# Kernel tuning notes

Hardware: AMD Instinct MI355X
Metric: run time of the kernel (lower is better)

The kernel has to match this reference:

```python
import jax, jax.numpy as jnp
import numpy as np

DIM = 1024
NUM_HEADS = 16
HEAD_DIM = DIM // NUM_HEADS
SCALE = HEAD_DIM ** (-0.5)


def setup_inputs() -> dict:
    key = jax.random.key(0)
    k_x, k_qkv, k_ow, k_ob = jax.random.split(key, 4)
    x = jax.random.normal(k_x, (4, 2048, DIM), dtype=jnp.float32)
    # nn.Linear(dim, 3*dim, bias=False): store as [dim, 3*dim] for x @ W
    w_qkv = jax.random.normal(k_qkv, (DIM, 3 * DIM), dtype=jnp.float32) * (DIM ** -0.5)
    w_out = jax.random.normal(k_ow, (DIM, DIM), dtype=jnp.float32) * (DIM ** -0.5)
    b_out = jax.random.normal(k_ob, (DIM,), dtype=jnp.float32) * 0.02
    return {"x": x, "w_qkv": w_qkv, "w_out": w_out, "b_out": b_out}


def reference(x, w_qkv, w_out, b_out):
    B, S, D = x.shape
    H, Hd = NUM_HEADS, HEAD_DIM
    qkv = x @ w_qkv                                  # [B, S, 3*D]
    # rearrange 'b s (v h d) -> v b h s d'
    qkv = qkv.reshape(B, S, 3, H, Hd).transpose(2, 0, 3, 1, 4)
    q, k, v = qkv[0], qkv[1], qkv[2]                 # each [B, H, S, Hd]
    scores = jnp.einsum('bhqd,bhkd->bhqk', q, k) * SCALE
    attn = jax.nn.softmax(scores, axis=-1)
    out = jnp.einsum('bhqk,bhkd->bhqd', attn, v)     # [B, H, S, Hd]
    out = out.transpose(0, 2, 1, 3).reshape(B, S, D)  # 'b h s d -> b s (h d)'
    return out @ w_out + b_out
```

## Files before the change

### kernel.cpp

```cpp
#include <hip/hip_runtime.h>
#include <hip/hip_bf16.h>
#include <stdint.h>

typedef __bf16 bf16_t;
typedef __bf16 bf16x4 __attribute__((ext_vector_type(4)));
typedef __bf16 bf16x8 __attribute__((ext_vector_type(8)));
typedef float f32x4 __attribute__((ext_vector_type(4)));
typedef unsigned short u16;

#define L2E 1.4426950408889634f
#define MC 69.249473f
#define QSC 0.18033688f

__device__ __forceinline__ void async_load16(const bf16_t* g, bf16_t* l) {
  __builtin_amdgcn_global_load_lds(
      (__attribute__((address_space(1))) uint32_t*)g,
      (__attribute__((address_space(3))) uint32_t*)l, 16, 0, 0);
}

__global__ void detect_k(const uint16_t* __restrict__ x, int* __restrict__ flag) {
  if (blockIdx.x != 0) return;
  const int lane = threadIdx.x & 63;
  int bad = 0;
#pragma unroll
  for (int p = 0; p < 4; ++p) {
    const int i = lane * 4 + p;
    uint16_t h = x[2 * i];
    int e = (h >> 7) & 0xFF;
    if (e == 0 || e >= 0xBD) bad++;
  }
  bad += __shfl_xor(bad, 1, 64);
  bad += __shfl_xor(bad, 2, 64);
  bad += __shfl_xor(bad, 4, 64);
  bad += __shfl_xor(bad, 8, 64);
  bad += __shfl_xor(bad, 16, 64);
  bad += __shfl_xor(bad, 32, 64);
  if (lane == 0 && threadIdx.x < 64) *flag = (bad > 32) ? 1 : 0;
}

__global__ void convert_k(const void* __restrict__ in, bf16_t* __restrict__ out,
                          int n, const int* __restrict__ flag) {
  const int f = *flag;
  const int i0 = blockIdx.x * blockDim.x + threadIdx.x;
  const int stride = gridDim.x * blockDim.x;
  if (f) {
    const float* p = (const float*)in;
    for (int i = i0; i < n; i += stride) {
      float v = p[i];
      v = (v == v) ? v : 0.f;
      v = fminf(fmaxf(v, -1e6f), 1e6f);
      out[i] = (bf16_t)v;
    }
  } else {
    const bf16_t* p = (const bf16_t*)in;
    for (int i = i0; i < n; i += stride) {
      float v = (float)p[i];
      v = (v == v) ? v : 0.f;
      v = fminf(fmaxf(v, -1e6f), 1e6f);
      out[i] = (bf16_t)v;
    }
  }
}

__global__ __launch_bounds__(256) void wtrans_k(const void* __restrict__ in,
                                                bf16_t* __restrict__ out, int R,
                                                int C, const int* __restrict__ flag) {
  __shared__ u16 tile[64][65];
  const int f = *flag;
  const int tr = blockIdx.y * 64, tc = blockIdx.x * 64;
  const int t = threadIdx.x;
#pragma unroll
  for (int i = 0; i < 16; ++i) {
    int idx = i * 256 + t, r = idx >> 6, c = idx & 63;
    float v;
    if (f)
      v = ((const float*)in)[(size_t)(tr + r) * C + tc + c];
    else
      v = (float)((const bf16_t*)in)[(size_t)(tr + r) * C + tc + c];
    v = (v == v) ? v : 0.f;
    v = fminf(fmaxf(v, -1e6f), 1e6f);
    bf16_t b = (bf16_t)v;
    tile[r][c] = *(u16*)&b;
  }
  __syncthreads();
#pragma unroll
  for (int i = 0; i < 16; ++i) {
    int idx = i * 256 + t, r = idx >> 6, c = idx & 63;
    ((u16*)out)[(size_t)(tc + r) * R + tr + c] = tile[c][r];
  }
}

__device__ __forceinline__ void gemm_bt_mainloop(
    const bf16_t* __restrict__ A, const bf16_t* __restrict__ Bt, int K, int m0,
    int n0, bf16_t* As, bf16_t* Bs, f32x4 acc[4][4]) {
  const int t = threadIdx.x, lane = t & 63, w = t >> 6;
  const int l15 = lane & 15, quad = lane >> 4;
  const int wm = (w >> 1) * 64, wn = (w & 1) * 64;
  const int srow = w * 16 + (lane >> 2);
  const int sk = (lane & 3) * 8;
  const bf16_t* gA = A + (size_t)(m0 + srow) * K + sk;
  const bf16_t* gB = Bt + (size_t)(n0 + srow) * K + sk;
  bf16_t* lA = As + w * 512;
  bf16_t* lB = Bs + w * 512;
  const size_t gstep = (size_t)64 * K;

  for (int kt = 0; kt < K; kt += 32) {
    __syncthreads();
    async_load16(gA, lA);
    async_load16(gA + gstep, lA + 2048);
    async_load16(gB, lB);
    async_load16(gB + gstep, lB + 2048);
    gA += 32;
    gB += 32;
    __syncthreads();
    bf16x8 af[4], bfr[4];
#pragma unroll
    for (int f = 0; f < 4; ++f) {
      af[f] = *(const bf16x8*)(As + (wm + f * 16 + l15) * 32 + quad * 8);
      bfr[f] = *(const bf16x8*)(Bs + (wn + f * 16 + l15) * 32 + quad * 8);
    }
#pragma unroll
    for (int i = 0; i < 4; ++i)
#pragma unroll
      for (int j = 0; j < 4; ++j)
        acc[i][j] =
            __builtin_amdgcn_mfma_f32_16x16x32_bf16(af[i], bfr[j], acc[i][j], 0, 0, 0);
  }
}

__global__ __launch_bounds__(256) void qkv_gemm_k(const bf16_t* __restrict__ X,
                                                  const bf16_t* __restrict__ WqT,
                                                  bf16_t* __restrict__ qo,
                                                  bf16_t* __restrict__ ko,
                                                  bf16_t* __restrict__ vto) {
  __shared__ __align__(16) bf16_t As[128 * 32];
  __shared__ __align__(16) bf16_t Bs[128 * 32];
  const int m0 = blockIdx.y * 128, n0 = blockIdx.x * 128;
  f32x4 acc[4][4];
  const f32x4 z = {0.f, 0.f, 0.f, 0.f};
#pragma unroll
  for (int i = 0; i < 4; ++i)
#pragma unroll
    for (int j = 0; j < 4; ++j) acc[i][j] = z;
  gemm_bt_mainloop(X, WqT, 1024, m0, n0, As, Bs, acc);

  const int lane = threadIdx.x & 63, w = threadIdx.x >> 6;
  const int l15 = lane & 15, quad = lane >> 4;
  const int wm = (w >> 1) * 64, wn = (w & 1) * 64;
#pragma unroll
  for (int j = 0; j < 4; ++j) {
    const int gnb = n0 + wn + j * 16;
    const int vi = gnb >> 10;
    const int rem = gnb & 1023;
    const int h = rem >> 6;
    const int d = (rem & 63) + l15;
    if (vi == 2) {
#pragma unroll
      for (int i = 0; i < 4; ++i) {
        const int gm0 = m0 + wm + i * 16 + quad * 4;
        const int b = gm0 >> 11, s = gm0 & 2047;
        bf16x4 pv;
#pragma unroll
        for (int r = 0; r < 4; ++r) pv[r] = (bf16_t)acc[i][j][r];
        *(bf16x4*)(vto + ((size_t)(b * 16 + h) * 64 + d) * 2048 + s) = pv;
      }
    } else {
      const float scale = (vi == 0) ? QSC : 1.0f;
      bf16_t* dst = (vi == 0) ? qo : ko;
#pragma unroll
      for (int i = 0; i < 4; ++i) {
#pragma unroll
        for (int r = 0; r < 4; ++r) {
          const int gm = m0 + wm + i * 16 + quad * 4 + r;
          const int b = gm >> 11, s = gm & 2047;
          dst[(((size_t)(b * 16 + h) * 2048 + s) << 6) + d] =
              (bf16_t)(acc[i][j][r] * scale);
        }
      }
    }
  }
}

__global__ __launch_bounds__(256) void out_gemm_k(const bf16_t* __restrict__ Ain,
                                                  const bf16_t* __restrict__ WoT,
                                                  const bf16_t* __restrict__ bias,
                                                  void* __restrict__ outp,
                                                  const int* __restrict__ flag) {
  __shared__ __align__(16) bf16_t As[128 * 32];
  __shared__ __align__(16) bf16_t Bs[128 * 32];
  const int m0 = blockIdx.y * 128, n0 = blockIdx.x * 128;
  f32x4 acc[4][4];
  const f32x4 z = {0.f, 0.f, 0.f, 0.f};
#pragma unroll
  for (int i = 0; i < 4; ++i)
#pragma unroll
    for (int j = 0; j < 4; ++j) acc[i][j] = z;
  gemm_bt_mainloop(Ain, WoT, 1024, m0, n0, As, Bs, acc);

  const int f32out = *flag;
  const int lane = threadIdx.x & 63, w = threadIdx.x >> 6;
  const int l15 = lane & 15, quad = lane >> 4;
  const int wm = (w >> 1) * 64, wn = (w & 1) * 64;
#pragma unroll
  for (int j = 0; j < 4; ++j) {
    const int gn = n0 + wn + j * 16 + l15;
    const float bv = (float)bias[gn];
#pragma unroll
    for (int i = 0; i < 4; ++i) {
#pragma unroll
      for (int r = 0; r < 4; ++r) {
        const int gm = m0 + wm + i * 16 + quad * 4 + r;
        const float val = acc[i][j][r] + bv;
        if (f32out)
          ((float*)outp)[(size_t)gm * 1024 + gn] = val;
        else
          ((bf16_t*)outp)[(size_t)gm * 1024 + gn] = (bf16_t)val;
      }
    }
  }
}

#define KTILE 4096

__global__ __launch_bounds__(256, 2) void attn_k(const bf16_t* __restrict__ q,
                                                 const bf16_t* __restrict__ k,
                                                 const bf16_t* __restrict__ vt,
                                                 bf16_t* __restrict__ o) {
  __shared__ __align__(16) bf16_t Ps[256 * 64];
  __shared__ __align__(16) bf16_t Ks[2 * KTILE];
  __shared__ __align__(16) bf16_t Vts[2 * KTILE];

  const int t = threadIdx.x, lane = t & 63, w = t >> 6;
  const int l15 = lane & 15, quad = lane >> 4;
  const int x = blockIdx.x;
  const int j = x >> 3;
  const int bh = (x & 7) * 8 + (j >> 3);
  const int qt = j & 7;
  const bf16_t* qp = q + ((size_t)bh * 2048 + qt * 256) * 64;
  const bf16_t* kp = k + (size_t)bh * 2048 * 64;
  const bf16_t* vp = vt + (size_t)bh * 64 * 2048;

  const int lane8 = lane >> 3, lc = lane & 7;
  int kOff[2], vOff[2], ldsOff[2];
#pragma unroll
  for (int c = 0; c < 2; ++c) {
    const int rho = (w * 2 + c) * 8 + lane8;
    const int srow = (rho >> 4) + (rho & 15) * 4;
    const int col = (lc ^ (rho & 7)) * 8;
    kOff[c] = srow * 64 + col;
    vOff[c] = rho * 2048 + col;
    ldsOff[c] = (w * 2 + c) * 512;
  }

#pragma unroll
  for (int c = 0; c < 2; ++c) {
    async_load16(kp + kOff[c], Ks + ldsOff[c]);
    async_load16(vp + vOff[c], Vts + ldsOff[c]);
  }
#pragma unroll
  for (int p = 0; p < 8; ++p) {
    const int off = p * 2048 + t * 8;
    async_load16(qp + off, Ps + off);
  }
  __syncthreads();

  bf16x8 qf[4][2];
#pragma unroll
  for (int qs = 0; qs < 4; ++qs)
#pragma unroll
    for (int ks = 0; ks < 2; ++ks)
      qf[qs][ks] = *(const bf16x8*)(Ps + (w * 64 + qs * 16 + l15) * 64 +
                                    ks * 32 + quad * 8);

  f32x4 acc[4][4], asum[4];
  const f32x4 z = {0.f, 0.f, 0.f, 0.f};
  const f32x4 minit = {-MC, -MC, -MC, -MC};
  bf16x8 onesf;
#pragma unroll
  for (int i = 0; i < 8; ++i) onesf[i] = (bf16_t)1.0f;
#pragma unroll
  for (int qs = 0; qs < 4; ++qs) {
    asum[qs] = z;
#pragma unroll
    for (int f = 0; f < 4; ++f) acc[qs][f] = z;
  }

  bf16_t* psw = Ps + w * 64 * 64;

  for (int kt = 0; kt < 32; ++kt) {
    const int b = kt & 1;
    if (kt < 31) {
      const int bn = b ^ 1;
#pragma unroll
      for (int c = 0; c < 2; ++c) {
        async_load16(kp + (size_t)(kt + 1) * KTILE + kOff[c],
                     Ks + bn * KTILE + ldsOff[c]);
        async_load16(vp + (size_t)(kt + 1) * 64 + vOff[c],
                     Vts + bn * KTILE + ldsOff[c]);
      }
    }

    const bf16_t* Kb = Ks + b * KTILE;
    const bf16_t* Vb = Vts + b * KTILE;

    f32x4 sacc[4][4];
    {
      const int cx = ((quad ^ (l15 & 7)) * 8);
      bf16x8 kf[4];
#pragma unroll
      for (int f = 0; f < 4; ++f)
        kf[f] = *(const bf16x8*)(Kb + (f * 16 + l15) * 64 + cx);
      __builtin_amdgcn_s_setprio(1);
#pragma unroll
      for (int qs = 0; qs < 4; ++qs)
#pragma unroll
        for (int f = 0; f < 4; ++f)
          sacc[qs][f] = __builtin_amdgcn_mfma_f32_16x16x32_bf16(
              qf[qs][0], kf[f], minit, 0, 0, 0);
      __builtin_amdgcn_s_setprio(0);
    }
    {
      const int cx = (((4 + quad) ^ (l15 & 7)) * 8);
      bf16x8 kf[4];
#pragma unroll
      for (int f = 0; f < 4; ++f)
        kf[f] = *(const bf16x8*)(Kb + (f * 16 + l15) * 64 + cx);
      __builtin_amdgcn_s_setprio(1);
#pragma unroll
      for (int qs = 0; qs < 4; ++qs)
#pragma unroll
        for (int f = 0; f < 4; ++f)
          sacc[qs][f] = __builtin_amdgcn_mfma_f32_16x16x32_bf16(
              qf[qs][1], kf[f], sacc[qs][f], 0, 0, 0);
      __builtin_amdgcn_s_setprio(0);
    }

#pragma unroll
    for (int qs = 0; qs < 4; ++qs)
#pragma unroll
      for (int r = 0; r < 4; ++r) {
        bf16x4 pk;
#pragma unroll
        for (int f = 0; f < 4; ++f)
          pk[f] =
              (bf16_t)__builtin_amdgcn_exp2f(fminf(sacc[qs][f][r], 0.f));
        const int row = qs * 16 + quad * 4 + r;
        *(bf16x4*)(psw + row * 64 + ((l15 >> 1) ^ (row & 7)) * 8 +
                   (l15 & 1) * 4) = pk;
      }

#pragma unroll
    for (int ks = 0; ks < 2; ++ks) {
      const int cx = (((ks * 4 + quad) ^ (l15 & 7)) * 8);
      bf16x8 vf[4];
#pragma unroll
      for (int f = 0; f < 4; ++f)
        vf[f] = *(const bf16x8*)(Vb + (f * 16 + l15) * 64 + cx);
#pragma unroll
      for (int qs = 0; qs < 4; ++qs) {
        bf16x8 pf = *(const bf16x8*)(psw + (qs * 16 + l15) * 64 +
                                     ((ks * 4 + quad) ^ (l15 & 7)) * 8);
        __builtin_amdgcn_s_setprio(1);
#pragma unroll
        for (int f = 0; f < 4; ++f)
          acc[qs][f] = __builtin_amdgcn_mfma_f32_16x16x32_bf16(
              pf, vf[f], acc[qs][f], 0, 0, 0);
        asum[qs] = __builtin_amdgcn_mfma_f32_16x16x32_bf16(pf, onesf, asum[qs],
                                                           0, 0, 0);
        __builtin_amdgcn_s_setprio(0);
      }
    }

    if (kt < 31) __syncthreads();
  }

  const int b = bh >> 4, h = bh & 15;
#pragma unroll
  for (int qs = 0; qs < 4; ++qs)
#pragma unroll
    for (int r = 0; r < 4; ++r) {
      const int srow = qt * 256 + w * 64 + qs * 16 + quad * 4 + r;
      const float inv = 1.0f / fmaxf(asum[qs][r], 1e-37f);
#pragma unroll
      for (int f = 0; f < 4; ++f) {
        const int d = f * 16 + l15;
        o[(size_t)(b * 2048 + srow) * 1024 + h * 64 + d] =
            (bf16_t)(acc[qs][f][r] * inv);
      }
    }
}

extern "C" void kernel_launch(void* const* d_in, const int* in_sizes, int n_in,
                              void* d_out, int out_size, void* d_ws, size_t ws_size,
                              hipStream_t stream) {
  const void* x_raw = d_in[0];
  const void* wqkv_raw = d_in[1];
  const void* wout_raw = d_in[2];
  const void* bout_raw = d_in[3];

  const int nx = 4 * 2048 * 1024;
  const int nwq = 1024 * 3072;
  const int nwo = 1024 * 1024;
  const int nb = 1024;

  char* ws = (char*)d_ws;
  int* flag = (int*)ws;
  bf16_t* xb = (bf16_t*)(ws + 256);
  bf16_t* wqbT = xb + nx;
  bf16_t* wobT = wqbT + nwq;
  bf16_t* bob = wobT + nwo;
  bf16_t* qb = bob + nb;
  const size_t bhsd = (size_t)4 * 16 * 2048 * 64;
  bf16_t* kb = qb + bhsd;
  bf16_t* vtb = kb + bhsd;
  bf16_t* ab = xb;

  detect_k<<<1, 64, 0, stream>>>((const uint16_t*)x_raw, flag);
  convert_k<<<2048, 256, 0, stream>>>(x_raw, xb, nx, flag);
  wtrans_k<<<dim3(3072 / 64, 1024 / 64), 256, 0, stream>>>(wqkv_raw, wqbT, 1024,
                                                           3072, flag);
  wtrans_k<<<dim3(1024 / 64, 1024 / 64), 256, 0, stream>>>(wout_raw, wobT, 1024,
                                                           1024, flag);
  convert_k<<<4, 256, 0, stream>>>(bout_raw, bob, nb, flag);

  qkv_gemm_k<<<dim3(3072 / 128, 8192 / 128), 256, 0, stream>>>(xb, wqbT, qb, kb,
                                                               vtb);
  attn_k<<<dim3(512), 256, 0, stream>>>(qb, kb, vtb, ab);
  out_gemm_k<<<dim3(1024 / 128, 8192 / 128), 256, 0, stream>>>(ab, wobT, bob,
                                                               d_out, flag);
}
```

Baseline: 291.6 us.

## Keep softmax probabilities in registers via lane shuffles instead of LDS

Removes the 32KB P staging buffer from shared memory. The QK^T MFMA operands are swapped so score outputs come out transposed, and the exp'd probabilities are packed to bf16 pairs and redistributed across lanes with shuffles to form the PV A-operand. Q is staged through the K/V buffers before the loop, which lowers LDS use and may raise occupancy. The cost is many ds_bpermute shuffles per tile plus a moved barrier at loop start.

```diff
diff --git a/kernel.cpp b/kernel.cpp
--- a/kernel.cpp
+++ b/kernel.cpp
@@ -6,6 +6,7 @@
 typedef __bf16 bf16x4 __attribute__((ext_vector_type(4)));
 typedef __bf16 bf16x8 __attribute__((ext_vector_type(8)));
 typedef float f32x4 __attribute__((ext_vector_type(4)));
+typedef unsigned int u32x4 __attribute__((ext_vector_type(4)));
 typedef unsigned short u16;
 
 #define L2E 1.4426950408889634f
@@ -16,6 +17,11 @@
   __builtin_amdgcn_global_load_lds(
       (__attribute__((address_space(1))) uint32_t*)g,
       (__attribute__((address_space(3))) uint32_t*)l, 16, 0, 0);
+}
+
+__device__ __forceinline__ uint32_t pack2(float lo, float hi) {
+  bf16_t l = (bf16_t)lo, h = (bf16_t)hi;
+  return (uint32_t)(*(u16*)&l) | ((uint32_t)(*(u16*)&h) << 16);
 }
 
 __global__ void detect_k(const uint16_t* __restrict__ x, int* __restrict__ flag) {
@@ -226,7 +232,6 @@
                                                  const bf16_t* __restrict__ k,
                                                  const bf16_t* __restrict__ vt,
                                                  bf16_t* __restrict__ o) {
-  __shared__ __align__(16) bf16_t Ps[256 * 64];
   __shared__ __align__(16) bf16_t Ks[2 * KTILE];
   __shared__ __align__(16) bf16_t Vts[2 * KTILE];
 
@@ -252,25 +257,40 @@
     ldsOff[c] = (w * 2 + c) * 512;
   }
 
+  {
+    const int qr = t >> 3, qc = t & 7;
+#pragma unroll
+    for (int p = 0; p < 4; ++p) {
+      const int r0 = p * 32 + qr;
+      const int r1 = 128 + r0;
+      async_load16(qp + (size_t)r0 * 64 + (qc ^ (r0 & 7)) * 8,
+                   Ks + r0 * 64 + qc * 8);
+      async_load16(qp + (size_t)r1 * 64 + (qc ^ (r1 & 7)) * 8,
+                   Vts + r0 * 64 + qc * 8);
+    }
+  }
+  __syncthreads();
+
+  bf16x8 qf[4][2];
+  {
+    const bf16_t* qarena = (w < 2) ? Ks : Vts;
+    const int wbase = (w & 1) * 64;
+#pragma unroll
+    for (int qs = 0; qs < 4; ++qs)
+#pragma unroll
+      for (int ks = 0; ks < 2; ++ks) {
+        const int row = wbase + qs * 16 + l15;
+        qf[qs][ks] = *(const bf16x8*)(qarena + row * 64 +
+                                      (((ks * 4 + quad) ^ (row & 7)) * 8));
+      }
+  }
+  __syncthreads();
+
 #pragma unroll
   for (int c = 0; c < 2; ++c) {
     async_load16(kp + kOff[c], Ks + ldsOff[c]);
     async_load16(vp + vOff[c], Vts + ldsOff[c]);
   }
-#pragma unroll
-  for (int p = 0; p < 8; ++p) {
-    const int off = p * 2048 + t * 8;
-    async_load16(qp + off, Ps + off);
-  }
-  __syncthreads();
-
-  bf16x8 qf[4][2];
-#pragma unroll
-  for (int qs = 0; qs < 4; ++qs)
-#pragma unroll
-    for (int ks = 0; ks < 2; ++ks)
-      qf[qs][ks] = *(const bf16x8*)(Ps + (w * 64 + qs * 16 + l15) * 64 +
-                                    ks * 32 + quad * 8);
 
   f32x4 acc[4][4], asum[4];
   const f32x4 z = {0.f, 0.f, 0.f, 0.f};
@@ -285,12 +305,10 @@
     for (int f = 0; f < 4; ++f) acc[qs][f] = z;
   }
 
-  bf16_t* psw = Ps + w * 64 * 64;
-
   for (int kt = 0; kt < 32; ++kt) {
-    const int b = kt & 1;
+    __syncthreads();
     if (kt < 31) {
-      const int bn = b ^ 1;
+      const int bn = (kt + 1) & 1;
 #pragma unroll
       for (int c = 0; c < 2; ++c) {
         async_load16(kp + (size_t)(kt + 1) * KTILE + kOff[c],
@@ -300,8 +318,8 @@
       }
     }
 
-    const bf16_t* Kb = Ks + b * KTILE;
-    const bf16_t* Vb = Vts + b * KTILE;
+    const bf16_t* Kb = Ks + (kt & 1) * KTILE;
+    const bf16_t* Vb = Vts + (kt & 1) * KTILE;
 
     f32x4 sacc[4][4];
     {
@@ -316,7 +334,7 @@
 #pragma unroll
         for (int f = 0; f < 4; ++f)
           sacc[qs][f] = __builtin_amdgcn_mfma_f32_16x16x32_bf16(
-              qf[qs][0], kf[f], minit, 0, 0, 0);
+              kf[f], qf[qs][0], minit, 0, 0, 0);
       __builtin_amdgcn_s_setprio(0);
     }
     {
@@ -331,35 +349,41 @@
 #pragma unroll
         for (int f = 0; f < 4; ++f)
           sacc[qs][f] = __builtin_amdgcn_mfma_f32_16x16x32_bf16(
-              qf[qs][1], kf[f], sacc[qs][f], 0, 0, 0);
+              kf[f], qf[qs][1], sacc[qs][f], 0, 0, 0);
       __builtin_amdgcn_s_setprio(0);
     }
 
+    uint32_t pk[4][8];
 #pragma unroll
     for (int qs = 0; qs < 4; ++qs)
 #pragma unroll
       for (int r = 0; r < 4; ++r) {
-        bf16x4 pk;
-#pragma unroll
-        for (int f = 0; f < 4; ++f)
-          pk[f] =
-              (bf16_t)__builtin_amdgcn_exp2f(fminf(sacc[qs][f][r], 0.f));
-        const int row = qs * 16 + quad * 4 + r;
-        *(bf16x4*)(psw + row * 64 + ((l15 >> 1) ^ (row & 7)) * 8 +
-                   (l15 & 1) * 4) = pk;
-      }
-
-#pragma unroll
-    for (int ks = 0; ks < 2; ++ks) {
-      const int cx = (((ks * 4 + quad) ^ (l15 & 7)) * 8);
+        const float e0 = __builtin_amdgcn_exp2f(fminf(sacc[qs][0][r], 0.f));
+        const float e1 = __builtin_amdgcn_exp2f(fminf(sacc[qs][1][r], 0.f));
+        const float e2 = __builtin_amdgcn_exp2f(fminf(sacc[qs][2][r], 0.f));
+        const float e3 = __builtin_amdgcn_exp2f(fminf(sacc[qs][3][r], 0.f));
+        pk[qs][2 * r] = pack2(e0, e1);
+        pk[qs][2 * r + 1] = pack2(e2, e3);
+      }
+
+#pragma unroll
+    for (int ks2 = 0; ks2 < 2; ++ks2) {
+      const int cx = (((ks2 * 4 + quad) ^ (l15 & 7)) * 8);
       bf16x8 vf[4];
 #pragma unroll
       for (int f = 0; f < 4; ++f)
         vf[f] = *(const bf16x8*)(Vb + (f * 16 + l15) * 64 + cx);
+      const int srcl = l15 + ((ks2 * 2 + (quad >> 1)) << 4);
 #pragma unroll
       for (int qs = 0; qs < 4; ++qs) {
-        bf16x8 pf = *(const bf16x8*)(psw + (qs * 16 + l15) * 64 +
-                                     ((ks * 4 + quad) ^ (l15 & 7)) * 8);
+        u32x4 av;
+#pragma unroll
+        for (int jj = 0; jj < 4; ++jj) {
+          const uint32_t lo = (uint32_t)__shfl((int)pk[qs][jj], srcl, 64);
+          const uint32_t hi = (uint32_t)__shfl((int)pk[qs][4 + jj], srcl, 64);
+          av[jj] = (quad & 1) ? hi : lo;
+        }
+        const bf16x8 pf = __builtin_bit_cast(bf16x8, av);
         __builtin_amdgcn_s_setprio(1);
 #pragma unroll
         for (int f = 0; f < 4; ++f)
@@ -370,8 +394,6 @@
         __builtin_amdgcn_s_setprio(0);
       }
     }
-
-    if (kt < 31) __syncthreads();
   }
 
   const int b = bh >> 4, h = bh & 15;
```

Result: slower. 315.1 us (+8.1%).

## Halve attention query tile to 128 rows and double grid for occupancy

Applied to the files above, without the earlier changes.

The attention kernel now processes 128 query rows per block (32 per wave) instead of 256, and launches 1024 blocks instead of 512. Q is staged through the K buffer with a swizzle, and the P buffer shrinks, which cuts LDS and register use so launch bounds can ask for 3 blocks per CU. The aim is better occupancy and CU load balance on the 256-CU device. In exchange, each K/V tile loaded into LDS is reused by half as many query rows, so K/V traffic doubles, and a barrier is added at the top of each iteration.

```diff
diff --git a/kernel.cpp b/kernel.cpp
--- a/kernel.cpp
+++ b/kernel.cpp
@@ -222,21 +222,21 @@
 
 #define KTILE 4096
 
-__global__ __launch_bounds__(256, 2) void attn_k(const bf16_t* __restrict__ q,
+__global__ __launch_bounds__(256, 3) void attn_k(const bf16_t* __restrict__ q,
                                                  const bf16_t* __restrict__ k,
                                                  const bf16_t* __restrict__ vt,
                                                  bf16_t* __restrict__ o) {
-  __shared__ __align__(16) bf16_t Ps[256 * 64];
   __shared__ __align__(16) bf16_t Ks[2 * KTILE];
   __shared__ __align__(16) bf16_t Vts[2 * KTILE];
+  __shared__ __align__(16) bf16_t Pb[4 * 32 * 64];
 
   const int t = threadIdx.x, lane = t & 63, w = t >> 6;
   const int l15 = lane & 15, quad = lane >> 4;
   const int x = blockIdx.x;
   const int j = x >> 3;
-  const int bh = (x & 7) * 8 + (j >> 3);
-  const int qt = j & 7;
-  const bf16_t* qp = q + ((size_t)bh * 2048 + qt * 256) * 64;
+  const int bh = (x & 7) * 8 + (j >> 4);
+  const int qt = j & 15;
+  const bf16_t* qp = q + ((size_t)bh * 2048 + qt * 128) * 64;
   const bf16_t* kp = k + (size_t)bh * 2048 * 64;
   const bf16_t* vp = vt + (size_t)bh * 64 * 2048;
 
@@ -252,45 +252,53 @@
     ldsOff[c] = (w * 2 + c) * 512;
   }
 
+  {
+    const int qr = t >> 3, qc = t & 7;
+#pragma unroll
+    for (int p = 0; p < 4; ++p) {
+      const int r0 = p * 32 + qr;
+      async_load16(qp + (size_t)r0 * 64 + (qc ^ (r0 & 7)) * 8,
+                   Ks + r0 * 64 + qc * 8);
+    }
+  }
+  __syncthreads();
+
+  bf16x8 qf[2][2];
+#pragma unroll
+  for (int qs = 0; qs < 2; ++qs)
+#pragma unroll
+    for (int ks = 0; ks < 2; ++ks) {
+      const int row = w * 32 + qs * 16 + l15;
+      qf[qs][ks] = *(const bf16x8*)(Ks + row * 64 +
+                                    (((ks * 4 + quad) ^ (row & 7)) * 8));
+    }
+  __syncthreads();
+
 #pragma unroll
   for (int c = 0; c < 2; ++c) {
     async_load16(kp + kOff[c], Ks + ldsOff[c]);
     async_load16(vp + vOff[c], Vts + ldsOff[c]);
   }
-#pragma unroll
-  for (int p = 0; p < 8; ++p) {
-    const int off = p * 2048 + t * 8;
-    async_load16(qp + off, Ps + off);
-  }
-  __syncthreads();
-
-  bf16x8 qf[4][2];
-#pragma unroll
-  for (int qs = 0; qs < 4; ++qs)
-#pragma unroll
-    for (int ks = 0; ks < 2; ++ks)
-      qf[qs][ks] = *(const bf16x8*)(Ps + (w * 64 + qs * 16 + l15) * 64 +
-                                    ks * 32 + quad * 8);
-
-  f32x4 acc[4][4], asum[4];
+
+  f32x4 acc[2][4], asum[2];
   const f32x4 z = {0.f, 0.f, 0.f, 0.f};
   const f32x4 minit = {-MC, -MC, -MC, -MC};
   bf16x8 onesf;
 #pragma unroll
   for (int i = 0; i < 8; ++i) onesf[i] = (bf16_t)1.0f;
 #pragma unroll
-  for (int qs = 0; qs < 4; ++qs) {
+  for (int qs = 0; qs < 2; ++qs) {
     asum[qs] = z;
 #pragma unroll
     for (int f = 0; f < 4; ++f) acc[qs][f] = z;
   }
 
-  bf16_t* psw = Ps + w * 64 * 64;
+  bf16_t* psw = Pb + w * 32 * 64;
 
   for (int kt = 0; kt < 32; ++kt) {
-    const int b = kt & 1;
+    __syncthreads();
     if (kt < 31) {
-      const int bn = b ^ 1;
+      const int bn = (kt + 1) & 1;
 #pragma unroll
       for (int c = 0; c < 2; ++c) {
         async_load16(kp + (size_t)(kt + 1) * KTILE + kOff[c],
@@ -300,10 +308,10 @@
       }
     }
 
-    const bf16_t* Kb = Ks + b * KTILE;
-    const bf16_t* Vb = Vts + b * KTILE;
-
-    f32x4 sacc[4][4];
+    const bf16_t* Kb = Ks + (kt & 1) * KTILE;
+    const bf16_t* Vb = Vts + (kt & 1) * KTILE;
+
+    f32x4 sacc[2][4];
     {
       const int cx = ((quad ^ (l15 & 7)) * 8);
       bf16x8 kf[4];
@@ -312,7 +320,7 @@
         kf[f] = *(const bf16x8*)(Kb + (f * 16 + l15) * 64 + cx);
       __builtin_amdgcn_s_setprio(1);
 #pragma unroll
-      for (int qs = 0; qs < 4; ++qs)
+      for (int qs = 0; qs < 2; ++qs)
 #pragma unroll
         for (int f = 0; f < 4; ++f)
           sacc[qs][f] = __builtin_amdgcn_mfma_f32_16x16x32_bf16(
@@ -327,7 +335,7 @@
         kf[f] = *(const bf16x8*)(Kb + (f * 16 + l15) * 64 + cx);
       __builtin_amdgcn_s_setprio(1);
 #pragma unroll
-      for (int qs = 0; qs < 4; ++qs)
+      for (int qs = 0; qs < 2; ++qs)
 #pragma unroll
         for (int f = 0; f < 4; ++f)
           sacc[qs][f] = __builtin_amdgcn_mfma_f32_16x16x32_bf16(
@@ -336,14 +344,13 @@
     }
 
 #pragma unroll
-    for (int qs = 0; qs < 4; ++qs)
+    for (int qs = 0; qs < 2; ++qs)
 #pragma unroll
       for (int r = 0; r < 4; ++r) {
         bf16x4 pk;
 #pragma unroll
         for (int f = 0; f < 4; ++f)
-          pk[f] =
-              (bf16_t)__builtin_amdgcn_exp2f(fminf(sacc[qs][f][r], 0.f));
+          pk[f] = (bf16_t)__builtin_amdgcn_exp2f(fminf(sacc[qs][f][r], 0.f));
         const int row = qs * 16 + quad * 4 + r;
         *(bf16x4*)(psw + row * 64 + ((l15 >> 1) ^ (row & 7)) * 8 +
                    (l15 & 1) * 4) = pk;
@@ -357,7 +364,7 @@
       for (int f = 0; f < 4; ++f)
         vf[f] = *(const bf16x8*)(Vb + (f * 16 + l15) * 64 + cx);
 #pragma unroll
-      for (int qs = 0; qs < 4; ++qs) {
+      for (int qs = 0; qs < 2; ++qs) {
         bf16x8 pf = *(const bf16x8*)(psw + (qs * 16 + l15) * 64 +
                                      ((ks * 4 + quad) ^ (l15 & 7)) * 8);
         __builtin_amdgcn_s_setprio(1);
@@ -370,16 +377,14 @@
         __builtin_amdgcn_s_setprio(0);
       }
     }
-
-    if (kt < 31) __syncthreads();
   }
 
   const int b = bh >> 4, h = bh & 15;
 #pragma unroll
-  for (int qs = 0; qs < 4; ++qs)
+  for (int qs = 0; qs < 2; ++qs)
 #pragma unroll
     for (int r = 0; r < 4; ++r) {
-      const int srow = qt * 256 + w * 64 + qs * 16 + quad * 4 + r;
+      const int srow = qt * 128 + w * 32 + qs * 16 + quad * 4 + r;
       const float inv = 1.0f / fmaxf(asum[qs][r], 1e-37f);
 #pragma unroll
       for (int f = 0; f < 4; ++f) {
@@ -425,7 +430,7 @@
 
   qkv_gemm_k<<<dim3(3072 / 128, 8192 / 128), 256, 0, stream>>>(xb, wqbT, qb, kb,
                                                                vtb);
-  attn_k<<<dim3(512), 256, 0, stream>>>(qb, kb, vtb, ab);
+  attn_k<<<dim3(1024), 256, 0, stream>>>(qb, kb, vtb, ab);
   out_gemm_k<<<dim3(1024 / 128, 8192 / 128), 256, 0, stream>>>(ab, wobT, bob,
                                                                d_out, flag);
 }
```

Result: slower. 298.9 us (+2.5%).
